# Optimization experiments

Hardware: AMD Instinct MI355X
Metric: run time of the kernel (lower is better)

The kernel has to match this reference:

```python
import jax, jax.numpy as jnp
import numpy as np

K_HEADS = 8
D_HEAD = 16
D_MODEL = K_HEADS * D_HEAD  # 128


def _xavier(key, shape):
    fan_in, fan_out = shape[0], shape[1]
    limit = (6.0 / (fan_in + fan_out)) ** 0.5
    return jax.random.uniform(key, shape, jnp.float32, -limit, limit)


def setup_inputs() -> dict:
    key = jax.random.key(0)
    ks = jax.random.split(key, 8)
    B, T, N = 8, 12, 512
    X = jax.random.normal(ks[0], (B, T, N, D_MODEL), jnp.float32)
    STE = jax.random.normal(ks[1], (B, T, N, 2 * D_MODEL), jnp.float32)
    Wq = _xavier(ks[2], (3 * D_MODEL, D_MODEL))
    Wk = _xavier(ks[3], (3 * D_MODEL, D_MODEL))
    Wv = _xavier(ks[4], (3 * D_MODEL, D_MODEL))
    Wo = _xavier(ks[5], (D_MODEL, D_MODEL))
    bq = jnp.zeros((D_MODEL,), jnp.float32)
    bk = jnp.zeros((D_MODEL,), jnp.float32)
    bv = jnp.zeros((D_MODEL,), jnp.float32)
    bo = jnp.zeros((D_MODEL,), jnp.float32)
    return {"X": X, "STE": STE, "Wq": Wq, "bq": bq, "Wk": Wk, "bk": bk,
            "Wv": Wv, "bv": bv, "Wo": Wo, "bo": bo}


def reference(X, STE, Wq, bq, Wk, bk, Wv, bv, Wo, bo):
    # 1x1-conv FCs == per-(t,node) linear + relu on the last dim
    H = jnp.concatenate([X, STE], axis=-1)              # [B,T,N,3D]
    q = jax.nn.relu(H @ Wq + bq)                        # [B,T,N,D]
    k = jax.nn.relu(H @ Wk + bk)
    v = jax.nn.relu(H @ Wv + bv)
    B, T, N, D = q.shape

    def heads(x):  # split last dim into K heads (head index major), move to front
        return x.reshape(B, T, N, K_HEADS, D_HEAD).transpose(3, 0, 1, 2, 4)

    qh, kh, vh = heads(q), heads(k), heads(v)           # [K,B,T,N,d]
    att = jnp.einsum('kbtnd,kbtmd->kbtnm', qh, kh) / (D_HEAD ** 0.5)
    att = jax.nn.softmax(att, axis=-1)                  # [K,B,T,N,N]
    o = jnp.einsum('kbtnm,kbtmd->kbtnd', att, vh)       # [K,B,T,N,d]
    o = o.transpose(1, 2, 3, 0, 4).reshape(B, T, N, D)  # concat heads on last dim
    return jax.nn.relu(o @ Wo + bo)
```

## Files before the change

kernel.cpp:

```cpp
#include <hip/hip_runtime.h>
#include <math.h>

constexpr int B_  = 8;
constexpr int T_  = 12;
constexpr int N_  = 512;
constexpr int DM  = 128;
constexpr int KH  = 8;
constexpr int DH  = 16;
constexpr int MR  = B_*T_*N_;
constexpr int K3  = 3*DM;
constexpr int TB  = 256;

typedef __attribute__((ext_vector_type(8))) short  bf16x8;
typedef __attribute__((ext_vector_type(4))) float  f32x4;
typedef __attribute__((ext_vector_type(4))) int    i32x4;

#define LOG2E 1.44269504088896340736f
#define SHIFT2 28.8539008177792681f

static __device__ inline float fast_exp2(float x) {
#if __has_builtin(__builtin_amdgcn_exp2f)
    return __builtin_amdgcn_exp2f(x);
#else
    return __expf(0.69314718055994531f * x);
#endif
}

static __device__ inline unsigned short f2bf(float x) {
    unsigned u = __float_as_uint(x);
    return (unsigned short)((u + 0x7fffu + ((u >> 16) & 1u)) >> 16);
}
static __device__ inline unsigned pk2(float a, float b) {
    unsigned ua = __float_as_uint(a) + 0x8000u;
    unsigned ub = __float_as_uint(b) + 0x8000u;
    return __builtin_amdgcn_perm(ub, ua, 0x07060302u);
}
static __device__ inline unsigned pk2t(float a, float b) {
    return __builtin_amdgcn_perm(__float_as_uint(b), __float_as_uint(a),
                                 0x07060302u);
}
static __device__ inline float fast_rcp(float x) {
#if __has_builtin(__builtin_amdgcn_rcpf)
    return __builtin_amdgcn_rcpf(x);
#else
    return 1.0f / x;
#endif
}

__global__ __launch_bounds__(256) void wprep_kernel(
    const float* __restrict__ Wq, const float* __restrict__ Wk,
    const float* __restrict__ Wv, const float* __restrict__ Wo,
    unsigned short* __restrict__ Wt, unsigned short* __restrict__ Wot)
{
    const int idx = blockIdx.x*256 + threadIdx.x;
    if (idx < 3*K3*DM) {
        const int p   = idx / (K3*DM);
        const int rem = idx - p*(K3*DM);
        const int k   = rem >> 7;
        const int n   = rem & 127;
        const float* W = (p == 0) ? Wq : ((p == 1) ? Wk : Wv);
        Wt[p*(K3*DM) + n*K3 + k] = f2bf(W[rem]);
    } else {
        const int i2 = idx - 3*K3*DM;
        const int k  = i2 >> 7;
        const int n  = i2 & 127;
        Wot[n*DM + k] = f2bf(Wo[i2]);
    }
}

__global__ __launch_bounds__(256, 2) void qkv_mfma(
    const float* __restrict__ X, const float* __restrict__ STE,
    const unsigned short* __restrict__ Wt,
    const float* __restrict__ bq, const float* __restrict__ bk,
    const float* __restrict__ bv,
    unsigned short* __restrict__ qb, unsigned short* __restrict__ kb2,
    unsigned short* __restrict__ vb2)
{
    __shared__ __align__(16) unsigned short Ash[128*72];
    __shared__ __align__(16) unsigned short Bsh[128*72];
    const int tid = threadIdx.x;
    const int rb  = blockIdx.x * 128;
    const int p   = blockIdx.y;
    const unsigned short* __restrict__ wtp = Wt + p*(K3*DM);
    const float* __restrict__ bias = (p == 0) ? bq : ((p == 1) ? bk : bv);
    unsigned short* __restrict__ outb = (p == 0) ? qb : ((p == 1) ? kb2 : vb2);
    const float scale = (p == 0) ? (0.25f * LOG2E) : 1.0f;

    const int lane = tid & 63, wv = tid >> 6;
    const int wm = (wv >> 1)*64, wn = (wv & 1)*64;
    const int m15 = lane & 15, g = lane >> 4;

    f32x4 acc[4][4] = {};

    for (int kt = 0; kt < K3; kt += 64) {
        const float* __restrict__ src = (kt < DM) ? (X + kt) : (STE + (kt - DM));
        const int ldr = (kt < DM) ? DM : 2*DM;
        #pragma unroll
        for (int i = 0; i < 8; ++i) {
            const int idx = tid + i*TB;
            const int m   = idx >> 4;
            const int c4  = idx & 15;
            const float4 f = *(const float4*)(src + (rb + m)*ldr + c4*4);
            uint2 d2;
            d2.x = pk2(f.x, f.y);
            d2.y = pk2(f.z, f.w);
            *(uint2*)(Ash + m*72 + c4*4) = d2;
        }
        #pragma unroll
        for (int i = 0; i < 4; ++i) {
            const int idx = tid + i*TB;
            const int n   = idx >> 3;
            const int kg  = idx & 7;
            *(uint4*)(Bsh + n*72 + kg*8) =
                *(const uint4*)(wtp + n*K3 + kt + kg*8);
        }
        __syncthreads();
        #pragma unroll
        for (int ks = 0; ks < 64; ks += 32) {
            bf16x8 af[4], bf[4];
            #pragma unroll
            for (int i = 0; i < 4; ++i)
                af[i] = *(const bf16x8*)(Ash + (wm + i*16 + m15)*72 + ks + g*8);
            #pragma unroll
            for (int j = 0; j < 4; ++j)
                bf[j] = *(const bf16x8*)(Bsh + (wn + j*16 + m15)*72 + ks + g*8);
            #pragma unroll
            for (int i = 0; i < 4; ++i)
                #pragma unroll
                for (int j = 0; j < 4; ++j)
                    acc[i][j] = __builtin_amdgcn_mfma_f32_16x16x32_bf16(
                        af[i], bf[j], acc[i][j], 0, 0, 0);
        }
        __syncthreads();
    }

    #pragma unroll
    for (int j = 0; j < 4; ++j) {
        const int c  = wn + j*16 + m15;
        const float bj = bias[c];
        const int h = c >> 4, d = c & 15;
        #pragma unroll
        for (int i = 0; i < 4; ++i) {
            #pragma unroll
            for (int r = 0; r < 4; ++r) {
                const int row = rb + wm + i*16 + g*4 + r;
                float v = acc[i][j][r] + bj;
                v = (v > 0.f ? v : 0.f) * scale;
                outb[(h*MR + row)*DH + d] = f2bf(v);
            }
        }
    }
}

__global__ __launch_bounds__(256, 3) void attn_kernel(
    const unsigned short* __restrict__ qb, const unsigned short* __restrict__ kb,
    const unsigned short* __restrict__ vb, unsigned short* __restrict__ ob)
{
    __shared__ __align__(16) unsigned short Klds[N_*DH];
    __shared__ __align__(16) unsigned short Vtlds[DH*536];

    const int tid = threadIdx.x;
    const int h   = blockIdx.x & (KH-1);
    const int bt  = blockIdx.x >> 3;
    const int base = (h*MR + bt*N_) * DH;

    {
        const uint4* kg = (const uint4*)(kb + base);
        uint4* kl = (uint4*)Klds;
        #pragma unroll
        for (int i = 0; i < 4; ++i) kl[tid + i*TB] = kg[tid + i*TB];
    }
    {
        const unsigned* vg = (const unsigned*)(vb + base);
        unsigned a[8], b[8];
        #pragma unroll
        for (int j = 0; j < 8; ++j) {
            a[j] = vg[(2*tid)*8 + j];
            b[j] = vg[(2*tid+1)*8 + j];
        }
        unsigned* vt = (unsigned*)Vtlds;
        #pragma unroll
        for (int d = 0; d < 16; ++d) {
            const int sh = (d & 1) * 16;
            const unsigned lo = (a[d >> 1] >> sh) & 0xffffu;
            const unsigned hi = (b[d >> 1] >> sh) & 0xffffu;
            vt[d*268 + tid] = lo | (hi << 16);
        }
    }
    __syncthreads();

    const int wv   = tid >> 6;
    const int lane = tid & 63;
    const int m    = lane & 15;
    const int g    = lane >> 4;

    bf16x8 qf[8];
    const unsigned short* qp = qb + base;
    #pragma unroll
    for (int j = 0; j < 8; ++j) {
        bf16x8 t = {0,0,0,0,0,0,0,0};
        if (g < 2) t = *(const bf16x8*)(qp + ((wv*8 + j)*16 + m)*DH + g*8);
        qf[j] = t;
    }

    const bf16x8 ones = {0x3F80,0x3F80,0x3F80,0x3F80,0x3F80,0x3F80,0x3F80,0x3F80};
    const f32x4 zshift = {-SHIFT2, -SHIFT2, -SHIFT2, -SHIFT2};

    f32x4 acc[8]  = {};
    f32x4 lacc[8] = {};

    for (int c = 0; c < 16; ++c) {
        const int kr0 = c*32 + ((m & 12) << 1) + (m & 3);
        bf16x8 kf0 = {0,0,0,0,0,0,0,0};
        bf16x8 kf1 = {0,0,0,0,0,0,0,0};
        if (g < 2) {
            kf0 = *(const bf16x8*)(Klds + kr0*DH + g*8);
            kf1 = *(const bf16x8*)(Klds + (kr0 + 4)*DH + g*8);
        }
        const bf16x8 vf = *(const bf16x8*)(Vtlds + m*536 + c*32 + g*8);

        #pragma unroll
        for (int j = 0; j < 8; ++j) {
            f32x4 s0 = __builtin_amdgcn_mfma_f32_16x16x32_bf16(kf0, qf[j], zshift, 0, 0, 0);
            f32x4 s1 = __builtin_amdgcn_mfma_f32_16x16x32_bf16(kf1, qf[j], zshift, 0, 0, 0);
            const float p0 = fast_exp2(s0[0]);
            const float p1 = fast_exp2(s0[1]);
            const float p2 = fast_exp2(s0[2]);
            const float p3 = fast_exp2(s0[3]);
            const float p4 = fast_exp2(s1[0]);
            const float p5 = fast_exp2(s1[1]);
            const float p6 = fast_exp2(s1[2]);
            const float p7 = fast_exp2(s1[3]);
            i32x4 pd = { (int)pk2t(p0, p1), (int)pk2t(p2, p3),
                         (int)pk2t(p4, p5), (int)pk2t(p6, p7) };
            const bf16x8 pf = __builtin_bit_cast(bf16x8, pd);
            acc[j]  = __builtin_amdgcn_mfma_f32_16x16x32_bf16(pf, vf,   acc[j],  0, 0, 0);
            lacc[j] = __builtin_amdgcn_mfma_f32_16x16x32_bf16(pf, ones, lacc[j], 0, 0, 0);
        }
    }

    #pragma unroll
    for (int j = 0; j < 8; ++j) {
        #pragma unroll
        for (int r = 0; r < 4; ++r) {
            const float iv = fast_rcp(lacc[j][r]);
            const int qrow = bt*N_ + (wv*8 + j)*16 + 4*g + r;
            ob[qrow*DM + h*DH + m] = f2bf(acc[j][r] * iv);
        }
    }
}

__global__ __launch_bounds__(256, 2) void out_mfma(
    const unsigned short* __restrict__ ot, const unsigned short* __restrict__ Wot,
    const float* __restrict__ bo, float* __restrict__ out)
{
    __shared__ __align__(16) unsigned short Ash[128*136];
    __shared__ __align__(16) unsigned short Bsh[128*136];
    const int tid = threadIdx.x;
    const int rb  = blockIdx.x * 128;
    const int lane = tid & 63, wv = tid >> 6;
    const int wm = (wv >> 1)*64, wn = (wv & 1)*64;
    const int m15 = lane & 15, g = lane >> 4;

    #pragma unroll
    for (int i = 0; i < 8; ++i) {
        const int idx = tid + i*TB;
        const int r  = idx >> 4;
        const int kg = idx & 15;
        *(uint4*)(Ash + r*136 + kg*8) = *(const uint4*)(ot + (rb + r)*DM + kg*8);
        *(uint4*)(Bsh + r*136 + kg*8) = *(const uint4*)(Wot + r*DM + kg*8);
    }
    __syncthreads();

    f32x4 acc[4][4] = {};
    #pragma unroll
    for (int ks = 0; ks < 128; ks += 32) {
        bf16x8 af[4], bf[4];
        #pragma unroll
        for (int i = 0; i < 4; ++i)
            af[i] = *(const bf16x8*)(Ash + (wm + i*16 + m15)*136 + ks + g*8);
        #pragma unroll
        for (int j = 0; j < 4; ++j)
            bf[j] = *(const bf16x8*)(Bsh + (wn + j*16 + m15)*136 + ks + g*8);
        #pragma unroll
        for (int i = 0; i < 4; ++i)
            #pragma unroll
            for (int j = 0; j < 4; ++j)
                acc[i][j] = __builtin_amdgcn_mfma_f32_16x16x32_bf16(
                    af[i], bf[j], acc[i][j], 0, 0, 0);
    }

    #pragma unroll
    for (int j = 0; j < 4; ++j) {
        const int c  = wn + j*16 + m15;
        const float bj = bo[c];
        #pragma unroll
        for (int i = 0; i < 4; ++i) {
            #pragma unroll
            for (int r = 0; r < 4; ++r) {
                const int row = rb + wm + i*16 + g*4 + r;
                float v = acc[i][j][r] + bj;
                out[row*DM + c] = v > 0.f ? v : 0.f;
            }
        }
    }
}

extern "C" void kernel_launch(void* const* d_in, const int* in_sizes, int n_in,
                              void* d_out, int out_size, void* d_ws, size_t ws_size,
                              hipStream_t stream)
{
    const float* X   = (const float*)d_in[0];
    const float* STE = (const float*)d_in[1];
    const float* Wq  = (const float*)d_in[2];
    const float* bq  = (const float*)d_in[3];
    const float* Wk  = (const float*)d_in[4];
    const float* bk  = (const float*)d_in[5];
    const float* Wv  = (const float*)d_in[6];
    const float* bv  = (const float*)d_in[7];
    const float* Wo  = (const float*)d_in[8];
    const float* bo  = (const float*)d_in[9];
    float* out = (float*)d_out;

    unsigned short* qb  = (unsigned short*)d_ws;
    unsigned short* kb  = qb  + (size_t)MR*DM;
    unsigned short* vb  = kb  + (size_t)MR*DM;
    unsigned short* ot  = vb  + (size_t)MR*DM;
    unsigned short* Wt  = ot  + (size_t)MR*DM;
    unsigned short* Wot = Wt  + (size_t)3*K3*DM;

    hipLaunchKernelGGL(wprep_kernel, dim3((3*K3*DM + DM*DM)/TB), dim3(TB), 0, stream,
                       Wq, Wk, Wv, Wo, Wt, Wot);
    hipLaunchKernelGGL(qkv_mfma, dim3(MR/128, 3), dim3(TB), 0, stream,
                       X, STE, Wt, bq, bk, bv, qb, kb, vb);
    hipLaunchKernelGGL(attn_kernel, dim3(KH*B_*T_), dim3(TB), 0, stream,
                       qb, kb, vb, ot);
    hipLaunchKernelGGL(out_mfma, dim3(MR/128), dim3(TB), 0, stream,
                       ot, Wot, bo, out);
}
```

Baseline: 189.0 us.

## Register-prefetch next K tile in QKV GEMM and raise occupancy hint

The QKV projection kernel now loads the next 64-wide K slice of X/STE and the weights into registers before running the MFMAs on the current slice, and converts and stores them to shared memory only at the start of the next iteration. This is meant to hide global-load latency behind the matrix math. It also raises launch_bounds min-blocks from 2 to 3. Together these raise register pressure (64 fp32 accumulators plus about 48 prefetch registers), which could cause spills under the tighter 3-block register limit.

```diff
diff --git a/kernel.cpp b/kernel.cpp
--- a/kernel.cpp
+++ b/kernel.cpp
@@ -68,7 +68,7 @@
     }
 }
 
-__global__ __launch_bounds__(256, 2) void qkv_mfma(
+__global__ __launch_bounds__(256, 3) void qkv_mfma(
     const float* __restrict__ X, const float* __restrict__ STE,
     const unsigned short* __restrict__ Wt,
     const float* __restrict__ bq, const float* __restrict__ bk,
@@ -90,9 +90,10 @@
     const int wm = (wv >> 1)*64, wn = (wv & 1)*64;
     const int m15 = lane & 15, g = lane >> 4;
 
-    f32x4 acc[4][4] = {};
-
-    for (int kt = 0; kt < K3; kt += 64) {
+    float4 aReg[8];
+    uint4  bReg[4];
+
+    auto LOADA = [&](int kt) {
         const float* __restrict__ src = (kt < DM) ? (X + kt) : (STE + (kt - DM));
         const int ldr = (kt < DM) ? DM : 2*DM;
         #pragma unroll
@@ -100,21 +101,49 @@
             const int idx = tid + i*TB;
             const int m   = idx >> 4;
             const int c4  = idx & 15;
-            const float4 f = *(const float4*)(src + (rb + m)*ldr + c4*4);
-            uint2 d2;
-            d2.x = pk2(f.x, f.y);
-            d2.y = pk2(f.z, f.w);
-            *(uint2*)(Ash + m*72 + c4*4) = d2;
-        }
+            aReg[i] = *(const float4*)(src + (rb + m)*ldr + c4*4);
+        }
+    };
+    auto LOADB = [&](int kt) {
         #pragma unroll
         for (int i = 0; i < 4; ++i) {
             const int idx = tid + i*TB;
             const int n   = idx >> 3;
             const int kg  = idx & 7;
-            *(uint4*)(Bsh + n*72 + kg*8) =
-                *(const uint4*)(wtp + n*K3 + kt + kg*8);
-        }
+            bReg[i] = *(const uint4*)(wtp + n*K3 + kt + kg*8);
+        }
+    };
+    auto STORE = [&]() {
+        #pragma unroll
+        for (int i = 0; i < 8; ++i) {
+            const int idx = tid + i*TB;
+            const int m   = idx >> 4;
+            const int c4  = idx & 15;
+            uint2 d2;
+            d2.x = pk2(aReg[i].x, aReg[i].y);
+            d2.y = pk2(aReg[i].z, aReg[i].w);
+            *(uint2*)(Ash + m*72 + c4*4) = d2;
+        }
+        #pragma unroll
+        for (int i = 0; i < 4; ++i) {
+            const int idx = tid + i*TB;
+            const int n   = idx >> 3;
+            const int kg  = idx & 7;
+            *(uint4*)(Bsh + n*72 + kg*8) = bReg[i];
+        }
+    };
+
+    f32x4 acc[4][4] = {};
+
+    LOADA(0); LOADB(0);
+    #pragma unroll
+    for (int kt = 0; kt < K3; kt += 64) {
+        STORE();
         __syncthreads();
+        if (kt + 64 < K3) {
+            LOADA(kt + 64);
+            LOADB(kt + 64);
+        }
         #pragma unroll
         for (int ks = 0; ks < 64; ks += 32) {
             bf16x8 af[4], bf[4];
```

Measured after the change: 244.4 us. 1.29x slower.

## Fuse Q/K/V projections into one kernel with fragment-packed weights

Applied to the files above, without the earlier changes.

The QKV projection now runs as a single kernel where each 64-row block computes all 384 output columns. This lets X and STE be read and converted to bf16 once instead of three times. Weights are pre-packed into MFMA fragment order so each lane loads B fragments straight from global memory without staging them in LDS. The A tile is double-buffered in LDS with register prefetch of the next k-slice. The trade-off is more accumulators per thread (24 MFMA tiles), a smaller row tile, and B fragments that go uncached through LDS.

```diff
diff --git a/kernel.cpp b/kernel.cpp
--- a/kernel.cpp
+++ b/kernel.cpp
@@ -50,7 +50,7 @@
 __global__ __launch_bounds__(256) void wprep_kernel(
     const float* __restrict__ Wq, const float* __restrict__ Wk,
     const float* __restrict__ Wv, const float* __restrict__ Wo,
-    unsigned short* __restrict__ Wt, unsigned short* __restrict__ Wot)
+    unsigned short* __restrict__ Wfrag, unsigned short* __restrict__ Wot)
 {
     const int idx = blockIdx.x*256 + threadIdx.x;
     if (idx < 3*K3*DM) {
@@ -59,7 +59,12 @@
         const int k   = rem >> 7;
         const int n   = rem & 127;
         const float* W = (p == 0) ? Wq : ((p == 1) ? Wk : Wv);
-        Wt[p*(K3*DM) + n*K3 + k] = f2bf(W[rem]);
+        const int c   = p*DM + n;
+        const int nb  = c >> 4, mm = c & 15;
+        const int ktI = k >> 6, kr = k & 63;
+        const int ksI = kr >> 5, gg = (kr >> 3) & 3, ee = kr & 7;
+        Wfrag[(((ktI*24 + nb)*2 + ksI) << 9) + ((gg*16 + mm) << 3) + ee]
+            = f2bf(W[rem]);
     } else {
         const int i2 = idx - 3*K3*DM;
         const int k  = i2 >> 7;
@@ -68,82 +73,93 @@
     }
 }
 
-__global__ __launch_bounds__(256, 2) void qkv_mfma(
+__global__ __launch_bounds__(256, 2) void qkv_fused(
     const float* __restrict__ X, const float* __restrict__ STE,
-    const unsigned short* __restrict__ Wt,
+    const unsigned short* __restrict__ Wfrag,
     const float* __restrict__ bq, const float* __restrict__ bk,
     const float* __restrict__ bv,
     unsigned short* __restrict__ qb, unsigned short* __restrict__ kb2,
     unsigned short* __restrict__ vb2)
 {
-    __shared__ __align__(16) unsigned short Ash[128*72];
-    __shared__ __align__(16) unsigned short Bsh[128*72];
+    __shared__ __align__(16) unsigned short Ash[2][64*72];
     const int tid = threadIdx.x;
-    const int rb  = blockIdx.x * 128;
-    const int p   = blockIdx.y;
-    const unsigned short* __restrict__ wtp = Wt + p*(K3*DM);
-    const float* __restrict__ bias = (p == 0) ? bq : ((p == 1) ? bk : bv);
-    unsigned short* __restrict__ outb = (p == 0) ? qb : ((p == 1) ? kb2 : vb2);
-    const float scale = (p == 0) ? (0.25f * LOG2E) : 1.0f;
+    const int rb  = blockIdx.x * 64;
 
     const int lane = tid & 63, wv = tid >> 6;
-    const int wm = (wv >> 1)*64, wn = (wv & 1)*64;
     const int m15 = lane & 15, g = lane >> 4;
 
-    f32x4 acc[4][4] = {};
-
-    for (int kt = 0; kt < K3; kt += 64) {
-        const float* __restrict__ src = (kt < DM) ? (X + kt) : (STE + (kt - DM));
-        const int ldr = (kt < DM) ? DM : 2*DM;
-        #pragma unroll
-        for (int i = 0; i < 8; ++i) {
-            const int idx = tid + i*TB;
-            const int m   = idx >> 4;
-            const int c4  = idx & 15;
-            const float4 f = *(const float4*)(src + (rb + m)*ldr + c4*4);
-            uint2 d2;
-            d2.x = pk2(f.x, f.y);
-            d2.y = pk2(f.z, f.w);
-            *(uint2*)(Ash + m*72 + c4*4) = d2;
-        }
-        #pragma unroll
-        for (int i = 0; i < 4; ++i) {
-            const int idx = tid + i*TB;
-            const int n   = idx >> 3;
-            const int kg  = idx & 7;
-            *(uint4*)(Bsh + n*72 + kg*8) =
-                *(const uint4*)(wtp + n*K3 + kt + kg*8);
-        }
+    const int am = tid >> 2;
+    const int ac = (tid & 3) * 4;
+    const int ar = tid >> 4;
+    const int ac4 = (tid & 15) * 4;
+
+    float4 a0, a1, a2, a3;
+
+#define QF_LOADA(kt_) {                                                      \
+        const float* __restrict__ asrc = ((kt_) < DM) ? (X + (kt_))          \
+                                                      : (STE + ((kt_) - DM));\
+        const int ldr = ((kt_) < DM) ? DM : 2*DM;                            \
+        const float* __restrict__ ap = asrc + (size_t)(rb + ar)*ldr + ac4;   \
+        a0 = *(const float4*)(ap           );                                \
+        a1 = *(const float4*)(ap + 16*ldr  );                                \
+        a2 = *(const float4*)(ap + 32*ldr  );                                \
+        a3 = *(const float4*)(ap + 48*ldr  ); }
+
+#define QF_STOREA(buf_) {                                                    \
+        unsigned short* Aw = Ash[buf_] + ar*72 + ac4;                        \
+        uint2 d;                                                             \
+        d.x = pk2(a0.x, a0.y); d.y = pk2(a0.z, a0.w); *(uint2*)(Aw        ) = d; \
+        d.x = pk2(a1.x, a1.y); d.y = pk2(a1.z, a1.w); *(uint2*)(Aw + 16*72) = d; \
+        d.x = pk2(a2.x, a2.y); d.y = pk2(a2.z, a2.w); *(uint2*)(Aw + 32*72) = d; \
+        d.x = pk2(a3.x, a3.y); d.y = pk2(a3.z, a3.w); *(uint2*)(Aw + 48*72) = d; }
+
+    f32x4 acc[4][6] = {};
+
+    const unsigned short* __restrict__ wlane = Wfrag + lane*8;
+
+    QF_LOADA(0);
+    QF_STOREA(0);
+
+    #pragma unroll
+    for (int ktI = 0; ktI < 6; ++ktI) {
+        const int cur = ktI & 1;
         __syncthreads();
-        #pragma unroll
-        for (int ks = 0; ks < 64; ks += 32) {
-            bf16x8 af[4], bf[4];
+        if (ktI < 5) { QF_LOADA((ktI + 1) * 64); }
+        #pragma unroll
+        for (int ksI = 0; ksI < 2; ++ksI) {
+            bf16x8 af[4], bfr[6];
             #pragma unroll
             for (int i = 0; i < 4; ++i)
-                af[i] = *(const bf16x8*)(Ash + (wm + i*16 + m15)*72 + ks + g*8);
-            #pragma unroll
-            for (int j = 0; j < 4; ++j)
-                bf[j] = *(const bf16x8*)(Bsh + (wn + j*16 + m15)*72 + ks + g*8);
+                af[i] = *(const bf16x8*)(Ash[cur] + (i*16 + m15)*72 + ksI*32 + g*8);
+            #pragma unroll
+            for (int j = 0; j < 6; ++j)
+                bfr[j] = *(const bf16x8*)(wlane +
+                          (size_t)(((ktI*24 + wv*6 + j)*2 + ksI) << 9));
             #pragma unroll
             for (int i = 0; i < 4; ++i)
                 #pragma unroll
-                for (int j = 0; j < 4; ++j)
+                for (int j = 0; j < 6; ++j)
                     acc[i][j] = __builtin_amdgcn_mfma_f32_16x16x32_bf16(
-                        af[i], bf[j], acc[i][j], 0, 0, 0);
-        }
-        __syncthreads();
-    }
-
-    #pragma unroll
-    for (int j = 0; j < 4; ++j) {
-        const int c  = wn + j*16 + m15;
-        const float bj = bias[c];
-        const int h = c >> 4, d = c & 15;
+                        af[i], bfr[j], acc[i][j], 0, 0, 0);
+        }
+        if (ktI < 5) { QF_STOREA(cur ^ 1); }
+    }
+
+    #pragma unroll
+    for (int j = 0; j < 6; ++j) {
+        const int c = wv*96 + j*16 + m15;
+        const int p = c >> 7;
+        const int n = c & 127;
+        const float* __restrict__ bias = (p == 0) ? bq : ((p == 1) ? bk : bv);
+        unsigned short* __restrict__ outb = (p == 0) ? qb : ((p == 1) ? kb2 : vb2);
+        const float scale = (p == 0) ? (0.25f * LOG2E) : 1.0f;
+        const float bj = bias[n];
+        const int h = n >> 4, d = n & 15;
         #pragma unroll
         for (int i = 0; i < 4; ++i) {
             #pragma unroll
             for (int r = 0; r < 4; ++r) {
-                const int row = rb + wm + i*16 + g*4 + r;
+                const int row = rb + i*16 + g*4 + r;
                 float v = acc[i][j][r] + bj;
                 v = (v > 0.f ? v : 0.f) * scale;
                 outb[(h*MR + row)*DH + d] = f2bf(v);
@@ -331,7 +347,7 @@
 
     hipLaunchKernelGGL(wprep_kernel, dim3((3*K3*DM + DM*DM)/TB), dim3(TB), 0, stream,
                        Wq, Wk, Wv, Wo, Wt, Wot);
-    hipLaunchKernelGGL(qkv_mfma, dim3(MR/128, 3), dim3(TB), 0, stream,
+    hipLaunchKernelGGL(qkv_fused, dim3(MR/64), dim3(TB), 0, stream,
                        X, STE, Wt, bq, bk, bv, qb, kb, vb);
     hipLaunchKernelGGL(attn_kernel, dim3(KH*B_*T_), dim3(TB), 0, stream,
                        qb, kb, vb, ot);
```

Result: no change. 191.9 us (+1.6%).
